# Kernel optimization log

Hardware: AMD Instinct MI355X
Metric: run time of the kernel (lower is better)

## Reference

```python
import jax, jax.numpy as jnp
import numpy as np

B, S, D, H = 4, 2048, 1024, 16
HD = D // H
DFF = 4 * D
NUM_LAYERS = 12
RES = 1.0 / float(np.sqrt(NUM_LAYERS))
SCALE = 1.0 / float(np.sqrt(D))  # module divides by sqrt(embed_dim), not head_dim
EPS = 1e-5


def setup_inputs() -> dict:
    key = jax.random.key(0)
    ks = jax.random.split(key, 12)
    s = 0.02
    p = lambda k, shp: (jax.random.normal(k, shp, jnp.float32) * s)
    return {
        "x": jax.random.normal(ks[0], (B, S, D), jnp.float32),
        "Wq": p(ks[1], (D, D)), "bq": jnp.zeros((D,), jnp.float32),
        "Wk": p(ks[2], (D, D)), "bk": jnp.zeros((D,), jnp.float32),
        "Wv": p(ks[3], (D, D)), "bv": jnp.zeros((D,), jnp.float32),
        "Wo": p(ks[4], (D, D)), "bo": jnp.zeros((D,), jnp.float32),
        "g1": jnp.ones((D,), jnp.float32), "be1": jnp.zeros((D,), jnp.float32),
        "g2": jnp.ones((D,), jnp.float32), "be2": jnp.zeros((D,), jnp.float32),
        "W1": p(ks[5], (D, DFF)), "b1": jnp.zeros((DFF,), jnp.float32),
        "W2": p(ks[6], (DFF, D)), "b2": jnp.zeros((D,), jnp.float32),
    }


def _layernorm(x, g, b):
    m = jnp.mean(x, axis=-1, keepdims=True)
    v = jnp.mean((x - m) ** 2, axis=-1, keepdims=True)
    return (x - m) * jax.lax.rsqrt(v + EPS) * g + b


def _attention(x, Wq, bq, Wk, bk, Wv, bv, Wo, bo):
    b, s, d = x.shape
    q = (x @ Wq + bq).reshape(b, s, H, HD)
    k = (x @ Wk + bk).reshape(b, s, H, HD)
    v = (x @ Wv + bv).reshape(b, s, H, HD)
    scores = jnp.einsum('bqhd,bkhd->bhqk', q, k) * SCALE  # [B,H,S,S]
    mask = jnp.tril(jnp.ones((s, s), dtype=bool))
    scores = jnp.where(mask, scores, -jnp.inf)
    attn = jax.nn.softmax(scores, axis=-1)  # dropout_rate=0 -> identity
    out = jnp.einsum('bhqk,bkhd->bqhd', attn, v).reshape(b, s, d)
    return out @ Wo + bo


def reference(x, Wq, bq, Wk, bk, Wv, bv, Wo, bo, g1, be1, g2, be2, W1, b1, W2, b2):
    x = x + RES * _attention(_layernorm(x, g1, be1), Wq, bq, Wk, bk, Wv, bv, Wo, bo)
    h = _layernorm(x, g2, be2)
    ffn = jax.nn.relu(h @ W1 + b1) @ W2 + b2
    x = x + RES * ffn
    return x
```

## Files before the change

### kernel.cpp

```cpp
#include <hip/hip_runtime.h>

typedef unsigned short ushort_t;
typedef unsigned int uint32;
typedef __attribute__((ext_vector_type(4))) float f32x4;
typedef __attribute__((ext_vector_type(8))) short bf16x8;

#define B_   4
#define S_   2048
#define D_   1024
#define H_   16
#define HD_  64
#define DFF_ 4096
#define M_   (B_ * S_)

#define RES_   0.28867513459481287f
#define SCALE_ 0.03125f
#define EPS_   1e-5f
#define LOG2E_ 1.4426950408889634f

__device__ __forceinline__ ushort_t f2bf(float f) {
    union { float f; uint32 u; } c; c.f = f;
    uint32 u = c.u + 0x7fffu + ((c.u >> 16) & 1u);
    return (ushort_t)(u >> 16);
}
__device__ __forceinline__ float bf2f(ushort_t h) {
    union { uint32 u; float f; } c; c.u = ((uint32)h) << 16;
    return c.f;
}
__device__ __forceinline__ float fexp2(float x) {
    float r; asm("v_exp_f32 %0, %1" : "=v"(r) : "v"(x)); return r;
}
__device__ __forceinline__ uint32 cvt_pk_bf16(float lo, float hi) {
    uint32 r;
    asm("v_cvt_pk_bf16_f32 %0, %1, %2" : "=v"(r) : "v"(lo), "v"(hi));
    return r;
}

#define GLDS(src_, dst_)                                                     \
    __builtin_amdgcn_global_load_lds(                                        \
        (const __attribute__((address_space(1))) void*)(src_),               \
        (__attribute__((address_space(3))) void*)(dst_), 16, 0, 0)

__global__ __launch_bounds__(256) void prep_kernel(
    const float* __restrict__ Wq, const float* __restrict__ Wk,
    const float* __restrict__ Wv, const float* __restrict__ Wo,
    const float* __restrict__ W1, const float* __restrict__ W2,
    const float* __restrict__ bq, const float* __restrict__ bk,
    const float* __restrict__ bv,
    ushort_t* __restrict__ Wqkvt, ushort_t* __restrict__ Wot,
    ushort_t* __restrict__ W1t, ushort_t* __restrict__ W2t,
    float* __restrict__ bqkv)
{
    __shared__ float tile[32][33];
    const int blk = blockIdx.x;
    const int tx = threadIdx.x;
    const int ty = threadIdx.y;

    if (blk >= 12288) {
        const int i = (blk - 12288) * 256 + ty * 32 + tx;
        if (i < 3 * D_) {
            float v = (i < D_) ? bq[i] : (i < 2 * D_) ? bk[i - D_] : bv[i - 2 * D_];
            bqkv[i] = v;
        }
        return;
    }

    const float* W; ushort_t* Wt; int K, N, bxi, byi;
    if (blk < 4096) {
        const int which = blk >> 10, local = blk & 1023;
        K = D_; N = D_;
        bxi = local & 31; byi = local >> 5;
        if (which == 0)      { W = Wq; Wt = Wqkvt; }
        else if (which == 1) { W = Wk; Wt = Wqkvt + D_ * D_; }
        else if (which == 2) { W = Wv; Wt = Wqkvt + 2 * D_ * D_; }
        else                 { W = Wo; Wt = Wot; }
    } else if (blk < 8192) {
        const int local = blk - 4096;
        W = W1; Wt = W1t; K = D_; N = DFF_;
        bxi = local & 127; byi = local >> 7;
    } else {
        const int local = blk - 8192;
        W = W2; Wt = W2t; K = DFF_; N = D_;
        bxi = local & 31; byi = local >> 5;
    }

    const int bx = bxi * 32;
    const int by = byi * 32;
    #pragma unroll
    for (int i = 0; i < 32; i += 8)
        tile[ty + i][tx] = W[(size_t)(by + ty + i) * N + bx + tx];
    __syncthreads();
    #pragma unroll
    for (int i = 0; i < 32; i += 8)
        Wt[(size_t)(bx + ty + i) * K + by + tx] = f2bf(tile[tx][ty + i]);
}

__global__ __launch_bounds__(256) void ln_kernel(
    const float* __restrict__ x, const float* __restrict__ g,
    const float* __restrict__ be, ushort_t* __restrict__ out)
{
    const int row = blockIdx.x;
    const int t = threadIdx.x;
    const int lane = t & 63;
    const int wave = t >> 6;
    const float4* xr = (const float4*)(x + (size_t)row * D_);
    float4 v = xr[t];
    float s  = v.x + v.y + v.z + v.w;
    float s2 = v.x * v.x + v.y * v.y + v.z * v.z + v.w * v.w;
    #pragma unroll
    for (int off = 32; off; off >>= 1) {
        s  += __shfl_xor(s, off);
        s2 += __shfl_xor(s2, off);
    }
    __shared__ float red[8];
    if (lane == 0) { red[wave * 2] = s; red[wave * 2 + 1] = s2; }
    __syncthreads();
    s  = red[0] + red[2] + red[4] + red[6];
    s2 = red[1] + red[3] + red[5] + red[7];
    const float mean = s * (1.0f / D_);
    const float var  = s2 * (1.0f / D_) - mean * mean;
    const float rstd = rsqrtf(var + EPS_);
    const float4 gv  = ((const float4*)g)[t];
    const float4 bv  = ((const float4*)be)[t];
    ushort_t o[4];
    o[0] = f2bf((v.x - mean) * rstd * gv.x + bv.x);
    o[1] = f2bf((v.y - mean) * rstd * gv.y + bv.y);
    o[2] = f2bf((v.z - mean) * rstd * gv.z + bv.z);
    o[3] = f2bf((v.w - mean) * rstd * gv.w + bv.w);
    *(ushort2*)&out[(size_t)row * D_ + t * 4]     = make_ushort2(o[0], o[1]);
    *(ushort2*)&out[(size_t)row * D_ + t * 4 + 2] = make_ushort2(o[2], o[3]);
}

__global__ __launch_bounds__(256) void vtrans_kernel(
    const ushort_t* __restrict__ qkv, ushort_t* __restrict__ vt)
{
    __shared__ __align__(16) ushort_t T[256 * 64];
    const int tid  = threadIdx.x;
    const int sblk = blockIdx.x & 7;
    const int bh   = blockIdx.x >> 3;
    const int b = bh >> 4, h = bh & 15;
    const ushort_t* src = qkv + (size_t)(b * S_ + sblk * 256) * (3 * D_) + 2 * D_ + h * 64;
    #pragma unroll
    for (int p = 0; p < 8; ++p) {
        const int L = p * 256 + tid;
        const int s = L >> 3, c = L & 7;
        bf16x8 v = *(const bf16x8*)(src + (size_t)s * (3 * D_) + c * 8);
        *(bf16x8*)&T[s * 64 + ((c ^ (s & 7)) << 3)] = v;
    }
    __syncthreads();
    #pragma unroll
    for (int p = 0; p < 8; ++p) {
        const int L = p * 256 + tid;
        const int hd = L >> 5, scn = L & 31;
        ushort_t tmp[8];
        #pragma unroll
        for (int j = 0; j < 8; ++j) {
            const int s = scn * 8 + j;
            tmp[j] = T[s * 64 + (((hd >> 3) ^ (s & 7)) << 3) + (hd & 7)];
        }
        *(bf16x8*)&vt[((size_t)bh * 64 + hd) * S_ + sblk * 256 + scn * 8] =
            *(const bf16x8*)tmp;
    }
}

template <int MODE>
__global__ __launch_bounds__(512, 2) void gemmT_kernel(
    const ushort_t* __restrict__ A, const ushort_t* __restrict__ Bt,
    const float* __restrict__ bias, const float* __restrict__ res,
    void* __restrict__ Cout, int M, int N, int K, int gx)
{
    constexpr int LOADS = 3;

    __shared__ __align__(16) ushort_t As[3][128 * 32];
    __shared__ __align__(16) ushort_t Bs[3][256 * 32];

    const int tid  = threadIdx.x;
    const int w    = tid >> 6;
    const int lane = tid & 63;
    const int l15  = lane & 15;
    const int g    = lane >> 4;

    const int cpx = gridDim.x >> 3;
    const int swz = (blockIdx.x & 7) * cpx + (blockIdx.x >> 3);
    const int bx = swz % gx, by = swz / gx;
    const int m0 = by * 128, n0 = bx * 256;

    const int wm = (w >> 2) * 64;
    const int wn = (w & 3) * 64;

    const ushort_t* srcA;
    int ldsA;
    const ushort_t* srcB[2];
    int ldsB[2];
    {
        const int L = tid;
        const int row = L >> 2;
        srcA = A + (size_t)(m0 + row) * K + (((L & 3) ^ ((row >> 1) & 3)) << 3);
        ldsA = (w * 64) * 8;
    }
    #pragma unroll
    for (int p = 0; p < 2; ++p) {
        const int L = p * 512 + tid;
        const int row = L >> 2;
        srcB[p] = Bt + (size_t)(n0 + row) * K + (((L & 3) ^ ((row >> 1) & 3)) << 3);
        ldsB[p] = (p * 512 + w * 64) * 8;
    }

    #define STAGE(koff_, buf_)                                               \
        do {                                                                 \
            GLDS(srcA + (koff_), &As[buf_][ldsA]);                           \
            GLDS(srcB[0] + (koff_), &Bs[buf_][ldsB[0]]);                     \
            GLDS(srcB[1] + (koff_), &Bs[buf_][ldsB[1]]);                     \
        } while (0)

    #define LDA(mf_) (*(const bf16x8*)&As[cur][(wm + (mf_) * 16 + l15) * 32 + \
                        ((g ^ (((wm + (mf_) * 16 + l15) >> 1) & 3)) << 3)])
    #define LDB(nf_) (*(const bf16x8*)&Bs[cur][(wn + (nf_) * 16 + l15) * 32 + \
                        ((g ^ (((wn + (nf_) * 16 + l15) >> 1) & 3)) << 3)])

    f32x4 acc[4][4] = {};
    const int NT = K >> 5;

    STAGE(0, 0);
    STAGE(32, 1);
    asm volatile("s_waitcnt vmcnt(%0)" :: "n"(LOADS) : "memory");
    __builtin_amdgcn_s_barrier();

    for (int t = 0; t < NT; ++t) {
        const int cur = t % 3;
        const bool more = (t + 2 < NT);
        const size_t koff = (size_t)(t + 2) * 32;

        bf16x8 af[4], bfr[4];
        #pragma unroll
        for (int nf = 0; nf < 4; ++nf) bfr[nf] = LDB(nf);
        #pragma unroll
        for (int mf = 0; mf < 4; ++mf) af[mf] = LDA(mf);

        if (more) STAGE(koff, (t + 2) % 3);
        __builtin_amdgcn_s_setprio(1);
        #pragma unroll
        for (int mf = 0; mf < 4; ++mf)
            #pragma unroll
            for (int nf = 0; nf < 4; ++nf)
                acc[mf][nf] = __builtin_amdgcn_mfma_f32_16x16x32_bf16(
                    af[mf], bfr[nf], acc[mf][nf], 0, 0, 0);
        __builtin_amdgcn_s_setprio(0);
        if (more)
            asm volatile("s_waitcnt vmcnt(%0)" :: "n"(LOADS) : "memory");
        else
            asm volatile("s_waitcnt vmcnt(0)" ::: "memory");
        __builtin_amdgcn_s_barrier();
    }
    #undef STAGE
    #undef LDA
    #undef LDB

    const int rbase = g * 4;
    #pragma unroll
    for (int mf = 0; mf < 4; ++mf) {
        #pragma unroll
        for (int nf = 0; nf < 4; ++nf) {
            const int col = n0 + wn + nf * 16 + l15;
            const float bcol = bias[col];
            #pragma unroll
            for (int r = 0; r < 4; ++r) {
                const int row = m0 + wm + mf * 16 + rbase + r;
                float v = acc[mf][nf][r] + bcol;
                const size_t idx = (size_t)row * N + col;
                if (MODE == 0) {
                    ((ushort_t*)Cout)[idx] = f2bf(v);
                } else if (MODE == 1) {
                    ((ushort_t*)Cout)[idx] = f2bf(fmaxf(v, 0.0f));
                } else {
                    ((float*)Cout)[idx] = res[idx] + RES_ * v;
                }
            }
        }
    }
}

__global__ __launch_bounds__(256) void fattn_kernel(
    const ushort_t* __restrict__ qkv, const ushort_t* __restrict__ vtg,
    ushort_t* __restrict__ out)
{
    __shared__ __align__(16) ushort_t Ks[2][64 * 64];
    __shared__ __align__(16) ushort_t Vt[2][64 * 64];
    __shared__ __align__(16) ushort_t Ps[4][16 * 64];

    const int tid  = threadIdx.x;
    const int lane = tid & 63;
    const int w    = tid >> 6;
    const int lin  = blockIdx.x;
    const int xi   = lin >> 6;
    const int bh   = lin & 63;
    const int b = bh >> 4, h = bh & 15;

    const int l15 = lane & 15;
    const int g   = lane >> 4;

    const size_t rs = 3 * D_;
    const ushort_t* Qg = qkv + (size_t)b * S_ * rs + h * HD_;
    const ushort_t* Kg = Qg + D_;
    const ushort_t* Vg = vtg + (size_t)bh * HD_ * S_;

    const int srow = tid >> 3;
    const int sc   = tid & 7;

    #pragma unroll
    for (int half = 0; half < 2; ++half) {
        const int qt = half ? xi : (S_ / 64 - 1) - xi;
        const int q0 = qt * 64;
        const int nkb = qt + 1;

        bf16x8 qf[2];
        {
            const int qrow = q0 + w * 16 + l15;
            #pragma unroll
            for (int kk = 0; kk < 2; ++kk) {
                bf16x8 tq = *(const bf16x8*)(Qg + (size_t)qrow * rs + kk * 32 + g * 8);
                #pragma unroll
                for (int e = 0; e < 8; ++e)
                    tq[e] = (short)f2bf(bf2f((ushort_t)tq[e]) * (SCALE_ * LOG2E_));
                qf[kk] = tq;
            }
        }

        float lrow = 0.f;
        f32x4 oacc[4] = {};

        bf16x8 kvreg[2][2], vvreg[2][2];
        #pragma unroll
        for (int p = 0; p < 2; ++p) {
            const int row = p * 32 + srow;
            kvreg[0][p] = *(const bf16x8*)(Kg + (size_t)row * rs + sc * 8);
            vvreg[0][p] = *(const bf16x8*)(Vg + (size_t)row * S_ + sc * 8);
        }
        if (nkb > 1) {
            #pragma unroll
            for (int p = 0; p < 2; ++p) {
                const int row = p * 32 + srow;
                kvreg[1][p] = *(const bf16x8*)(Kg + (size_t)(64 + row) * rs + sc * 8);
                vvreg[1][p] = *(const bf16x8*)(Vg + (size_t)row * S_ + 64 + sc * 8);
            }
        }

        int kb = 0;
        for (; kb + 1 < nkb; kb += 2) {
            __syncthreads();
            #pragma unroll
            for (int s = 0; s < 2; ++s)
                #pragma unroll
                for (int p = 0; p < 2; ++p) {
                    const int row = p * 32 + srow;
                    *(bf16x8*)&Ks[s][row * 64 + ((sc ^ (row & 7)) << 3)] = kvreg[s][p];
                    *(bf16x8*)&Vt[s][row * 64 + ((sc ^ (row & 7)) << 3)] = vvreg[s][p];
                }
            if (kb + 2 < nkb) {
                #pragma unroll
                for (int p = 0; p < 2; ++p) {
                    const int row = p * 32 + srow;
                    kvreg[0][p] = *(const bf16x8*)(
                        Kg + (size_t)((kb + 2) * 64 + row) * rs + sc * 8);
                    vvreg[0][p] = *(const bf16x8*)(
                        Vg + (size_t)row * S_ + (kb + 2) * 64 + sc * 8);
                }
            }
            if (kb + 3 < nkb) {
                #pragma unroll
                for (int p = 0; p < 2; ++p) {
                    const int row = p * 32 + srow;
                    kvreg[1][p] = *(const bf16x8*)(
                        Kg + (size_t)((kb + 3) * 64 + row) * rs + sc * 8);
                    vvreg[1][p] = *(const bf16x8*)(
                        Vg + (size_t)row * S_ + (kb + 3) * 64 + sc * 8);
                }
            }
            __syncthreads();

            f32x4 sf0[4] = {}, sf1[4] = {};
            __builtin_amdgcn_s_setprio(1);
            #pragma unroll
            for (int kk = 0; kk < 2; ++kk) {
                const int cc = kk * 4 + g;
                #pragma unroll
                for (int nf = 0; nf < 4; ++nf) {
                    const int keyr = nf * 16 + l15;
                    const int ko = keyr * 64 + ((cc ^ (keyr & 7)) << 3);
                    bf16x8 kf0 = *(const bf16x8*)&Ks[0][ko];
                    bf16x8 kf1 = *(const bf16x8*)&Ks[1][ko];
                    sf0[nf] = __builtin_amdgcn_mfma_f32_16x16x32_bf16(kf0, qf[kk], sf0[nf], 0, 0, 0);
                    sf1[nf] = __builtin_amdgcn_mfma_f32_16x16x32_bf16(kf1, qf[kk], sf1[nf], 0, 0, 0);
                }
            }
            __builtin_amdgcn_s_setprio(0);

            if (kb + 1 == nkb - 1) {
                const int q = q0 + w * 16 + l15;
                #pragma unroll
                for (int nf = 0; nf < 4; ++nf)
                    #pragma unroll
                    for (int r = 0; r < 4; ++r)
                        if ((kb + 1) * 64 + nf * 16 + g * 4 + r > q) sf1[nf][r] = -1e30f;
            }

            const int qrow = l15;
            #pragma unroll
            for (int s = 0; s < 2; ++s) {
                const f32x4* sfp = s ? sf1 : sf0;
                #pragma unroll
                for (int nf = 0; nf < 4; ++nf) {
                    const float p0 = fexp2(sfp[nf][0]);
                    const float p1 = fexp2(sfp[nf][1]);
                    const float p2 = fexp2(sfp[nf][2]);
                    const float p3 = fexp2(sfp[nf][3]);
                    lrow += (p0 + p1) + (p2 + p3);
                    uint2 pk = make_uint2(cvt_pk_bf16(p0, p1), cvt_pk_bf16(p2, p3));
                    const int c16 = ((nf << 1) + (g >> 1)) ^ (qrow & 7);
                    *(uint2*)((char*)Ps[w] + qrow * 128 + c16 * 16 + (g & 1) * 8) = pk;
                }
                #pragma unroll
                for (int kk = 0; kk < 2; ++kk) {
                    const int cc = kk * 4 + g;
                    const int c16 = cc ^ (qrow & 7);
                    bf16x8 pa = *(const bf16x8*)((const char*)Ps[w] + qrow * 128 + c16 * 16);
                    __builtin_amdgcn_s_setprio(1);
                    #pragma unroll
                    for (int nf = 0; nf < 4; ++nf) {
                        const int dr = nf * 16 + l15;
                        bf16x8 vf = *(const bf16x8*)&Vt[s][dr * 64 + ((cc ^ (dr & 7)) << 3)];
                        oacc[nf] = __builtin_amdgcn_mfma_f32_16x16x32_bf16(pa, vf, oacc[nf], 0, 0, 0);
                    }
                    __builtin_amdgcn_s_setprio(0);
                }
            }
        }

        if (kb < nkb) {
            __syncthreads();
            #pragma unroll
            for (int p = 0; p < 2; ++p) {
                const int row = p * 32 + srow;
                *(bf16x8*)&Ks[0][row * 64 + ((sc ^ (row & 7)) << 3)] = kvreg[0][p];
                *(bf16x8*)&Vt[0][row * 64 + ((sc ^ (row & 7)) << 3)] = vvreg[0][p];
            }
            __syncthreads();

            f32x4 sf0[4] = {};
            __builtin_amdgcn_s_setprio(1);
            #pragma unroll
            for (int kk = 0; kk < 2; ++kk) {
                const int cc = kk * 4 + g;
                #pragma unroll
                for (int nf = 0; nf < 4; ++nf) {
                    const int keyr = nf * 16 + l15;
                    bf16x8 kf = *(const bf16x8*)&Ks[0][keyr * 64 + ((cc ^ (keyr & 7)) << 3)];
                    sf0[nf] = __builtin_amdgcn_mfma_f32_16x16x32_bf16(kf, qf[kk], sf0[nf], 0, 0, 0);
                }
            }
            __builtin_amdgcn_s_setprio(0);

            {
                const int q = q0 + w * 16 + l15;
                #pragma unroll
                for (int nf = 0; nf < 4; ++nf)
                    #pragma unroll
                    for (int r = 0; r < 4; ++r)
                        if (kb * 64 + nf * 16 + g * 4 + r > q) sf0[nf][r] = -1e30f;
            }

            const int qrow = l15;
            #pragma unroll
            for (int nf = 0; nf < 4; ++nf) {
                const float p0 = fexp2(sf0[nf][0]);
                const float p1 = fexp2(sf0[nf][1]);
                const float p2 = fexp2(sf0[nf][2]);
                const float p3 = fexp2(sf0[nf][3]);
                lrow += (p0 + p1) + (p2 + p3);
                uint2 pk = make_uint2(cvt_pk_bf16(p0, p1), cvt_pk_bf16(p2, p3));
                const int c16 = ((nf << 1) + (g >> 1)) ^ (qrow & 7);
                *(uint2*)((char*)Ps[w] + qrow * 128 + c16 * 16 + (g & 1) * 8) = pk;
            }
            #pragma unroll
            for (int kk = 0; kk < 2; ++kk) {
                const int cc = kk * 4 + g;
                const int c16 = cc ^ (qrow & 7);
                bf16x8 pa = *(const bf16x8*)((const char*)Ps[w] + qrow * 128 + c16 * 16);
                __builtin_amdgcn_s_setprio(1);
                #pragma unroll
                for (int nf = 0; nf < 4; ++nf) {
                    const int dr = nf * 16 + l15;
                    bf16x8 vf = *(const bf16x8*)&Vt[0][dr * 64 + ((cc ^ (dr & 7)) << 3)];
                    oacc[nf] = __builtin_amdgcn_mfma_f32_16x16x32_bf16(pa, vf, oacc[nf], 0, 0, 0);
                }
                __builtin_amdgcn_s_setprio(0);
            }
        }

        lrow += __shfl_xor(lrow, 16);
        lrow += __shfl_xor(lrow, 32);
        const float linv = 1.0f / lrow;
        #pragma unroll
        for (int r = 0; r < 4; ++r) {
            const float li = __shfl(linv, g * 4 + r, 16);
            const int q = q0 + w * 16 + g * 4 + r;
            ushort_t* op = out + (size_t)(b * S_ + q) * D_ + h * HD_;
            #pragma unroll
            for (int nf = 0; nf < 4; ++nf)
                op[nf * 16 + l15] = f2bf(oacc[nf][r] * li);
        }
    }
}

extern "C" void kernel_launch(void* const* d_in, const int* in_sizes, int n_in,
                              void* d_out, int out_size, void* d_ws, size_t ws_size,
                              hipStream_t stream)
{
    const float* x   = (const float*)d_in[0];
    const float* Wq  = (const float*)d_in[1];
    const float* bq  = (const float*)d_in[2];
    const float* Wk  = (const float*)d_in[3];
    const float* bk  = (const float*)d_in[4];
    const float* Wv  = (const float*)d_in[5];
    const float* bv  = (const float*)d_in[6];
    const float* Wo  = (const float*)d_in[7];
    const float* bo  = (const float*)d_in[8];
    const float* g1  = (const float*)d_in[9];
    const float* be1 = (const float*)d_in[10];
    const float* g2  = (const float*)d_in[11];
    const float* be2 = (const float*)d_in[12];
    const float* W1  = (const float*)d_in[13];
    const float* b1  = (const float*)d_in[14];
    const float* W2  = (const float*)d_in[15];
    const float* b2  = (const float*)d_in[16];
    float* out = (float*)d_out;

    char* ws = (char*)d_ws;
    size_t o = 0;
    auto alloc = [&](size_t bytes) { size_t r = o; o = (o + bytes + 255) & ~(size_t)255; return r; };
    ushort_t* Wqkvt = (ushort_t*)(ws + alloc((size_t)3 * D_ * D_ * 2));
    ushort_t* Wot   = (ushort_t*)(ws + alloc((size_t)D_ * D_ * 2));
    ushort_t* W1t   = (ushort_t*)(ws + alloc((size_t)DFF_ * D_ * 2));
    ushort_t* W2t   = (ushort_t*)(ws + alloc((size_t)D_ * DFF_ * 2));
    float*    bqkv  = (float*)(ws + alloc((size_t)3 * D_ * 4));
    ushort_t* lnbuf = (ushort_t*)(ws + alloc((size_t)M_ * D_ * 2));
    ushort_t* bigbuf= (ushort_t*)(ws + alloc((size_t)M_ * DFF_ * 2));
    ushort_t* attnb = (ushort_t*)(ws + alloc((size_t)M_ * D_ * 2));
    float*    x1    = (float*)(ws + alloc((size_t)M_ * D_ * 4));
    ushort_t* vtbuf = (ushort_t*)(ws + alloc((size_t)M_ * D_ * 2));

    prep_kernel<<<12300, dim3(32, 8), 0, stream>>>(
        Wq, Wk, Wv, Wo, W1, W2, bq, bk, bv, Wqkvt, Wot, W1t, W2t, bqkv);

    ln_kernel<<<M_, 256, 0, stream>>>(x, g1, be1, lnbuf);
    gemmT_kernel<0><<<(M_/128)*(3*D_/256), 512, 0, stream>>>(
        lnbuf, Wqkvt, bqkv, nullptr, bigbuf, M_, 3*D_, D_, 3*D_/256);
    vtrans_kernel<<<512, 256, 0, stream>>>(bigbuf, vtbuf);
    fattn_kernel<<<(S_/128) * 64, 256, 0, stream>>>(bigbuf, vtbuf, attnb);
    gemmT_kernel<2><<<(M_/128)*(D_/256), 512, 0, stream>>>(
        attnb, Wot, bo, x, x1, M_, D_, D_, D_/256);
    ln_kernel<<<M_, 256, 0, stream>>>(x1, g2, be2, lnbuf);
    gemmT_kernel<1><<<(M_/128)*(DFF_/256), 512, 0, stream>>>(
        lnbuf, W1t, b1, nullptr, bigbuf, M_, DFF_, D_, DFF_/256);
    gemmT_kernel<2><<<(M_/128)*(D_/256), 512, 0, stream>>>(
        bigbuf, W2t, b2, x1, out, M_, D_, DFF_, D_/256);
}
```

Baseline: 363.6 us.

## Fuse first layernorm into weight-prep kernel and store residual intermediate in bf16

The first layernorm is merged into the weight transpose/convert kernel as extra blocks, which removes one launch and lets both independent jobs run concurrently. The intermediate residual x1 is now stored as bf16 rather than fp32, halving its write and two reads (second layernorm and final residual add). The cost is a rounding step on the residual stream before the final output, which loses precision and could affect tolerance.

Result: faster. 352.9 us, median of 2 (-2.9%).

```diff
diff --git a/kernel.cpp b/kernel.cpp
--- a/kernel.cpp
+++ b/kernel.cpp
@@ -41,23 +41,62 @@
         (const __attribute__((address_space(1))) void*)(src_),               \
         (__attribute__((address_space(3))) void*)(dst_), 16, 0, 0)
 
-__global__ __launch_bounds__(256) void prep_kernel(
+__global__ __launch_bounds__(256) void prepln_kernel(
+    const float* __restrict__ x, const float* __restrict__ g1,
+    const float* __restrict__ be1,
     const float* __restrict__ Wq, const float* __restrict__ Wk,
     const float* __restrict__ Wv, const float* __restrict__ Wo,
     const float* __restrict__ W1, const float* __restrict__ W2,
     const float* __restrict__ bq, const float* __restrict__ bk,
     const float* __restrict__ bv,
+    ushort_t* __restrict__ lnbuf,
     ushort_t* __restrict__ Wqkvt, ushort_t* __restrict__ Wot,
     ushort_t* __restrict__ W1t, ushort_t* __restrict__ W2t,
     float* __restrict__ bqkv)
 {
     __shared__ float tile[32][33];
+    __shared__ float red[8];
     const int blk = blockIdx.x;
-    const int tx = threadIdx.x;
-    const int ty = threadIdx.y;
-
-    if (blk >= 12288) {
-        const int i = (blk - 12288) * 256 + ty * 32 + tx;
+    const int tid = threadIdx.x;
+
+    if (blk < 8192) {
+        const int row = blk;
+        const int t = tid;
+        const int lane = t & 63;
+        const int wave = t >> 6;
+        float4 v = *((const float4*)x + (size_t)row * 256 + t);
+        float s  = v.x + v.y + v.z + v.w;
+        float s2 = v.x * v.x + v.y * v.y + v.z * v.z + v.w * v.w;
+        #pragma unroll
+        for (int off = 32; off; off >>= 1) {
+            s  += __shfl_xor(s, off);
+            s2 += __shfl_xor(s2, off);
+        }
+        if (lane == 0) { red[wave * 2] = s; red[wave * 2 + 1] = s2; }
+        __syncthreads();
+        s  = red[0] + red[2] + red[4] + red[6];
+        s2 = red[1] + red[3] + red[5] + red[7];
+        const float mean = s * (1.0f / D_);
+        const float var  = s2 * (1.0f / D_) - mean * mean;
+        const float rstd = rsqrtf(var + EPS_);
+        const float4 gv  = ((const float4*)g1)[t];
+        const float4 bvv = ((const float4*)be1)[t];
+        ushort_t o[4];
+        o[0] = f2bf((v.x - mean) * rstd * gv.x + bvv.x);
+        o[1] = f2bf((v.y - mean) * rstd * gv.y + bvv.y);
+        o[2] = f2bf((v.z - mean) * rstd * gv.z + bvv.z);
+        o[3] = f2bf((v.w - mean) * rstd * gv.w + bvv.w);
+        *(ushort2*)&lnbuf[(size_t)row * D_ + t * 4]     = make_ushort2(o[0], o[1]);
+        *(ushort2*)&lnbuf[(size_t)row * D_ + t * 4 + 2] = make_ushort2(o[2], o[3]);
+        return;
+    }
+
+    const int pb = blk - 8192;
+    const int tx = tid & 31;
+    const int ty = tid >> 5;
+
+    if (pb >= 12288) {
+        const int i = (pb - 12288) * 256 + tid;
         if (i < 3 * D_) {
             float v = (i < D_) ? bq[i] : (i < 2 * D_) ? bk[i - D_] : bv[i - 2 * D_];
             bqkv[i] = v;
@@ -66,20 +105,20 @@
     }
 
     const float* W; ushort_t* Wt; int K, N, bxi, byi;
-    if (blk < 4096) {
-        const int which = blk >> 10, local = blk & 1023;
+    if (pb < 4096) {
+        const int which = pb >> 10, local = pb & 1023;
         K = D_; N = D_;
         bxi = local & 31; byi = local >> 5;
         if (which == 0)      { W = Wq; Wt = Wqkvt; }
         else if (which == 1) { W = Wk; Wt = Wqkvt + D_ * D_; }
         else if (which == 2) { W = Wv; Wt = Wqkvt + 2 * D_ * D_; }
         else                 { W = Wo; Wt = Wot; }
-    } else if (blk < 8192) {
-        const int local = blk - 4096;
+    } else if (pb < 8192) {
+        const int local = pb - 4096;
         W = W1; Wt = W1t; K = D_; N = DFF_;
         bxi = local & 127; byi = local >> 7;
     } else {
-        const int local = blk - 8192;
+        const int local = pb - 8192;
         W = W2; Wt = W2t; K = DFF_; N = D_;
         bxi = local & 31; byi = local >> 5;
     }
@@ -95,16 +134,22 @@
         Wt[(size_t)(bx + ty + i) * K + by + tx] = f2bf(tile[tx][ty + i]);
 }
 
+template <int IN>
 __global__ __launch_bounds__(256) void ln_kernel(
-    const float* __restrict__ x, const float* __restrict__ g,
+    const void* __restrict__ xin, const float* __restrict__ g,
     const float* __restrict__ be, ushort_t* __restrict__ out)
 {
     const int row = blockIdx.x;
     const int t = threadIdx.x;
     const int lane = t & 63;
     const int wave = t >> 6;
-    const float4* xr = (const float4*)(x + (size_t)row * D_);
-    float4 v = xr[t];
+    float4 v;
+    if (IN) {
+        ushort4 u = *((const ushort4*)xin + (size_t)row * 256 + t);
+        v = make_float4(bf2f(u.x), bf2f(u.y), bf2f(u.z), bf2f(u.w));
+    } else {
+        v = *((const float4*)xin + (size_t)row * 256 + t);
+    }
     float s  = v.x + v.y + v.z + v.w;
     float s2 = v.x * v.x + v.y * v.y + v.z * v.z + v.w * v.w;
     #pragma unroll
@@ -166,7 +211,7 @@
 template <int MODE>
 __global__ __launch_bounds__(512, 2) void gemmT_kernel(
     const ushort_t* __restrict__ A, const ushort_t* __restrict__ Bt,
-    const float* __restrict__ bias, const float* __restrict__ res,
+    const float* __restrict__ bias, const void* __restrict__ res,
     void* __restrict__ Cout, int M, int N, int K, int gx)
 {
     constexpr int LOADS = 3;
@@ -272,8 +317,10 @@
                     ((ushort_t*)Cout)[idx] = f2bf(v);
                 } else if (MODE == 1) {
                     ((ushort_t*)Cout)[idx] = f2bf(fmaxf(v, 0.0f));
+                } else if (MODE == 3) {
+                    ((ushort_t*)Cout)[idx] = f2bf(((const float*)res)[idx] + RES_ * v);
                 } else {
-                    ((float*)Cout)[idx] = res[idx] + RES_ * v;
+                    ((float*)Cout)[idx] = bf2f(((const ushort_t*)res)[idx]) + RES_ * v;
                 }
             }
         }
@@ -546,22 +593,22 @@
     ushort_t* lnbuf = (ushort_t*)(ws + alloc((size_t)M_ * D_ * 2));
     ushort_t* bigbuf= (ushort_t*)(ws + alloc((size_t)M_ * DFF_ * 2));
     ushort_t* attnb = (ushort_t*)(ws + alloc((size_t)M_ * D_ * 2));
-    float*    x1    = (float*)(ws + alloc((size_t)M_ * D_ * 4));
+    ushort_t* x1b   = (ushort_t*)(ws + alloc((size_t)M_ * D_ * 2));
     ushort_t* vtbuf = (ushort_t*)(ws + alloc((size_t)M_ * D_ * 2));
 
-    prep_kernel<<<12300, dim3(32, 8), 0, stream>>>(
-        Wq, Wk, Wv, Wo, W1, W2, bq, bk, bv, Wqkvt, Wot, W1t, W2t, bqkv);
-
-    ln_kernel<<<M_, 256, 0, stream>>>(x, g1, be1, lnbuf);
+    prepln_kernel<<<20492, 256, 0, stream>>>(
+        x, g1, be1, Wq, Wk, Wv, Wo, W1, W2, bq, bk, bv,
+        lnbuf, Wqkvt, Wot, W1t, W2t, bqkv);
+
     gemmT_kernel<0><<<(M_/128)*(3*D_/256), 512, 0, stream>>>(
         lnbuf, Wqkvt, bqkv, nullptr, bigbuf, M_, 3*D_, D_, 3*D_/256);
     vtrans_kernel<<<512, 256, 0, stream>>>(bigbuf, vtbuf);
     fattn_kernel<<<(S_/128) * 64, 256, 0, stream>>>(bigbuf, vtbuf, attnb);
-    gemmT_kernel<2><<<(M_/128)*(D_/256), 512, 0, stream>>>(
-        attnb, Wot, bo, x, x1, M_, D_, D_, D_/256);
-    ln_kernel<<<M_, 256, 0, stream>>>(x1, g2, be2, lnbuf);
+    gemmT_kernel<3><<<(M_/128)*(D_/256), 512, 0, stream>>>(
+        attnb, Wot, bo, x, x1b, M_, D_, D_, D_/256);
+    ln_kernel<1><<<M_, 256, 0, stream>>>(x1b, g2, be2, lnbuf);
     gemmT_kernel<1><<<(M_/128)*(DFF_/256), 512, 0, stream>>>(
         lnbuf, W1t, b1, nullptr, bigbuf, M_, DFF_, D_, DFF_/256);
-    gemmT_kernel<2><<<(M_/128)*(D_/256), 512, 0, stream>>>(
-        bigbuf, W2t, b2, x1, out, M_, D_, DFF_, D_/256);
-}
+    gemmT_kernel<4><<<(M_/128)*(D_/256), 512, 0, stream>>>(
+        bigbuf, W2t, b2, x1b, out, M_, D_, DFF_, D_/256);
+}
```
